# Performance work log

Measured on AMD Instinct MI355X. Metric: run time of the kernel, lower is better.

Reference implementation:

```python
import jax, jax.numpy as jnp
import numpy as np
from jax import lax

N = 100000
IN_C, HID, OUT_C = 512, 256, 128
K_STEPS = 10
ALPHA = 0.1
RES_ALPHA = 1.0
LN_EPS = 1e-5


def layer_norm(h, g, b):
    mu = jnp.mean(h, axis=-1, keepdims=True)
    var = jnp.mean(jnp.square(h - mu), axis=-1, keepdims=True)
    return (h - mu) * lax.rsqrt(var + LN_EPS) * g + b


def appnp(h, src, dst):
    # add self loops
    loop = jnp.arange(N, dtype=src.dtype)
    s = jnp.concatenate([src, loop])
    d = jnp.concatenate([dst, loop])
    ew = jnp.ones(s.shape[0], h.dtype)
    deg = jax.ops.segment_sum(ew, d, num_segments=N)
    dis = jnp.where(deg > 0, lax.rsqrt(jnp.maximum(deg, 1e-12)), 0.0)
    norm = dis[s] * ew * dis[d]  # [E+N]
    h0 = h
    def step(carry, _):
        msg = norm[:, None] * carry[s]                      # gather [E+N, C]
        agg = jax.ops.segment_sum(msg, d, num_segments=N)    # scatter-add
        return (1.0 - ALPHA) * agg + ALPHA * h0, None
    h, _ = lax.scan(step, h, None, length=K_STEPS)
    return h


def setup_inputs() -> dict:
    key = jax.random.key(0)
    ks = jax.random.split(key, 12)
    def lin(k, fan_in, fan_out):
        bound = 1.0 / np.sqrt(fan_in)
        kw, kb = jax.random.split(k)
        W = jax.random.uniform(kw, (fan_in, fan_out), jnp.float32, -bound, bound)
        b = jax.random.uniform(kb, (fan_out,), jnp.float32, -bound, bound)
        return W, b
    x = jax.random.normal(ks[0], (N, IN_C), jnp.float32)
    edge_index = jax.random.randint(ks[1], (2, 1600000), 0, N, jnp.int32)
    W_in, b_in = lin(ks[2], IN_C, HID)
    W1, b1 = lin(ks[3], HID, HID)
    W2, b2 = lin(ks[4], HID, HID)
    W_out, b_out = lin(ks[5], HID, OUT_C)
    g1 = jnp.ones(HID); be1 = jnp.zeros(HID)
    g2 = jnp.ones(HID); be2 = jnp.zeros(HID)
    return {"x": x, "edge_index": edge_index,
            "W_in": W_in, "b_in": b_in,
            "W1": W1, "b1": b1, "g1": g1, "be1": be1,
            "W2": W2, "b2": b2, "g2": g2, "be2": be2,
            "W_out": W_out, "b_out": b_out}


def reference(x, edge_index, W_in, b_in, W1, b1, g1, be1, W2, b2, g2, be2, W_out, b_out):
    # MLP with residual blocks (eval mode: no dropout)
    h = x @ W_in + b_in
    for (W, b, g, be) in ((W1, b1, g1, be1), (W2, b2, g2, be2)):
        identity = h
        h = layer_norm(h @ W + b, g, be)
        h = RES_ALPHA * h + (1.0 - RES_ALPHA) * identity
        h = jax.nn.relu(h)
    h = h @ W_out + b_out
    # APPNP propagation
    return appnp(h, edge_index[0], edge_index[1])
```

## Files before the change

kernel.cpp:

```cpp
#include <hip/hip_runtime.h>

typedef unsigned short u16;
typedef unsigned long long u64;
typedef __attribute__((ext_vector_type(8))) short bfrag;
typedef __attribute__((ext_vector_type(4))) float f32x4;

__device__ inline float b2f(u16 u) {
    union { unsigned int i; float f; } v; v.i = ((unsigned int)u) << 16; return v.f;
}
__device__ inline u16 f2b(float f) {
    union { float f; unsigned int u; } v; v.f = f;
    unsigned int r = v.u + 0x7fffu + ((v.u >> 16) & 1u);
    return (u16)(r >> 16);
}
__device__ inline float ldF(const void* p, size_t i, bool bf) {
    return bf ? b2f(((const u16*)p)[i]) : ((const float*)p)[i];
}
__device__ inline void gload_lds16(const void* g, void* l) {
    __builtin_amdgcn_global_load_lds((const __attribute__((address_space(1))) unsigned int*)g,
                                     (__attribute__((address_space(3))) unsigned int*)l, 16, 0, 0);
}

__global__ void detect_k(const unsigned int* __restrict__ g1w, int* flag) {
    if (blockIdx.x == 0 && threadIdx.x == 0)
        *flag = (g1w[0] == 0x3F803F80u) ? 1 : 0;
}

__global__ void wt_k(const void* __restrict__ W, u16* __restrict__ Wt, int K, int NC,
                     const int* __restrict__ flagp) {
    int i = blockIdx.x * 256 + threadIdx.x;
    if (i >= K * NC) return;
    int k = i / NC, nn = i - k * NC;
    u16 v = (*flagp) ? ((const u16*)W)[i] : f2b(((const float*)W)[i]);
    Wt[(size_t)nn * K + k] = v;
}

template<int K, bool A_DUAL>
__global__ __launch_bounds__(256) void gemm_bt(const void* __restrict__ Ain, const u16* __restrict__ Bt,
                                               const void* __restrict__ bias, u16* __restrict__ C,
                                               int M, int NC, const int* __restrict__ flagp) {
    const int BM = 128, BN = 128, BK = 32;
    const int KI = K / BK;
    __shared__ u16 sh[32768];
    const bool bf = (*flagp != 0);
    int nt = NC / BN;

    int nwg = gridDim.x, bid = blockIdx.x;
    int qc = nwg >> 3, rc = nwg & 7;
    int xcd = bid & 7, off = bid >> 3;
    int swz = (xcd < rc ? xcd * (qc + 1) : rc * (qc + 1) + (xcd - rc) * qc) + off;
    int m0 = (swz / nt) * BM;
    int n0 = (swz % nt) * BN;

    int t = threadIdx.x;
    int lane = t & 63, wave = t >> 6;
    int wm = (wave >> 1) * 64, wn = (wave & 1) * 64;

    f32x4 acc[4][4];
#pragma unroll
    for (int i = 0; i < 4; i++)
#pragma unroll
        for (int j = 0; j < 4; j++) acc[i][j] = (f32x4){0.f, 0.f, 0.f, 0.f};

    char* shb = (char*)sh;
    auto ldsA = [&](int bufi) { return shb + bufi * 8192; };
    auto ldsB = [&](int bufi) { return shb + 32768 + bufi * 8192; };

    auto stageAsync = [&](int bufi, int kk) {
#pragma unroll
        for (int q = 0; q < 2; ++q) {
            int idx = q * 256 + t, row = idx >> 2, cb = (idx & 3) * 16;
            int ra = m0 + row; ra = ra < M ? ra : M - 1;
            gload_lds16((const char*)Bt + ((size_t)(n0 + row) * K + kk) * 2 + cb,
                        ldsB(bufi) + q * 4096 + wave * 1024);
            gload_lds16((const char*)Ain + ((size_t)ra * K + kk) * 2 + cb,
                        ldsA(bufi) + q * 4096 + wave * 1024);
        }
    };
    auto stageB = [&](int bufi, int kk) {
#pragma unroll
        for (int q = 0; q < 2; ++q) {
            int idx = q * 256 + t, row = idx >> 2, cb = (idx & 3) * 16;
            gload_lds16((const char*)Bt + ((size_t)(n0 + row) * K + kk) * 2 + cb,
                        ldsB(bufi) + q * 4096 + wave * 1024);
        }
    };
    float4 fr[2][2];
    auto loadA32 = [&](int kk) {
#pragma unroll
        for (int q = 0; q < 2; ++q) {
            int idx = q * 256 + t, row = idx >> 2, cf = (idx & 3) * 8;
            int ra = m0 + row; ra = ra < M ? ra : M - 1;
            const float* g = (const float*)Ain + (size_t)ra * K + kk + cf;
            fr[q][0] = *(const float4*)g;
            fr[q][1] = *(const float4*)(g + 4);
        }
    };
    auto writeA32 = [&](int bufi) {
#pragma unroll
        for (int q = 0; q < 2; ++q) {
            ushort4 o0, o1;
            o0.x = f2b(fr[q][0].x); o0.y = f2b(fr[q][0].y); o0.z = f2b(fr[q][0].z); o0.w = f2b(fr[q][0].w);
            o1.x = f2b(fr[q][1].x); o1.y = f2b(fr[q][1].y); o1.z = f2b(fr[q][1].z); o1.w = f2b(fr[q][1].w);
            char* la = ldsA(bufi) + q * 4096 + wave * 1024 + lane * 16;
            *(ushort4*)la = o0;
            *(ushort4*)(la + 8) = o1;
        }
    };

    int r16 = lane & 15, q8 = (lane >> 4) * 8;
    const bool a32 = A_DUAL && !bf;

    if (!a32) {
        stageAsync(0, 0);
        stageAsync(1, BK);
#pragma unroll
        for (int ki = 0; ki < KI; ++ki) {
            if (ki + 2 < KI) stageAsync((ki + 2) & 3, (ki + 2) * BK);
            if (ki + 2 < KI)       asm volatile("s_waitcnt vmcnt(8)" ::: "memory");
            else if (ki + 2 == KI) asm volatile("s_waitcnt vmcnt(4)" ::: "memory");
            else                   asm volatile("s_waitcnt vmcnt(0)" ::: "memory");
            asm volatile("s_barrier" ::: "memory");
            const u16* Ac = (const u16*)ldsA(ki & 3);
            const u16* Bc = (const u16*)ldsB(ki & 3);
            bfrag a[4], b[4];
#pragma unroll
            for (int i = 0; i < 4; i++) a[i] = *(const bfrag*)&Ac[(wm + i * 16 + r16) * BK + q8];
#pragma unroll
            for (int j = 0; j < 4; j++) b[j] = *(const bfrag*)&Bc[(wn + j * 16 + r16) * BK + q8];
#pragma unroll
            for (int i = 0; i < 4; i++)
#pragma unroll
                for (int j = 0; j < 4; j++)
                    acc[i][j] = __builtin_amdgcn_mfma_f32_16x16x32_bf16(a[i], b[j], acc[i][j], 0, 0, 0);
        }
    } else {
        loadA32(0);
        stageB(0, 0);
        writeA32(0);
        __syncthreads();
        int cur = 0;
        for (int k0 = 0; k0 < K; k0 += BK) {
            bool next = (k0 + BK < K);
            if (next) { loadA32(k0 + BK); stageB(cur ^ 1, k0 + BK); }
            const u16* Ac = (const u16*)ldsA(cur);
            const u16* Bc = (const u16*)ldsB(cur);
            bfrag a[4], b[4];
#pragma unroll
            for (int i = 0; i < 4; i++) a[i] = *(const bfrag*)&Ac[(wm + i * 16 + r16) * BK + q8];
#pragma unroll
            for (int j = 0; j < 4; j++) b[j] = *(const bfrag*)&Bc[(wn + j * 16 + r16) * BK + q8];
#pragma unroll
            for (int i = 0; i < 4; i++)
#pragma unroll
                for (int j = 0; j < 4; j++)
                    acc[i][j] = __builtin_amdgcn_mfma_f32_16x16x32_bf16(a[i], b[j], acc[i][j], 0, 0, 0);
            if (next) writeA32(cur ^ 1);
            __syncthreads();
            cur ^= 1;
        }
    }
    __syncthreads();

    int q4 = (lane >> 4) * 4;
#pragma unroll
    for (int j = 0; j < 4; j++) {
        int cg = n0 + wn + j * 16 + r16;
        float bvv = ldF(bias, cg, bf);
        int colb = (wn + j * 16 + r16) * 2;
#pragma unroll
        for (int i = 0; i < 4; i++) {
#pragma unroll
            for (int rr = 0; rr < 4; rr++) {
                int row = wm + i * 16 + q4 + rr;
                int sw = colb ^ (((row >> 2) & 3) << 5);
                *(u16*)(shb + row * 256 + sw) = f2b(acc[i][j][rr] + bvv);
            }
        }
    }
    __syncthreads();
#pragma unroll
    for (int pass = 0; pass < 8; ++pass) {
        int u = pass * 256 + t;
        int row = u >> 4;
        int cb = (u & 15) * 16;
        int sw = cb ^ (((row >> 2) & 3) << 5);
        uint4 vv = *(const uint4*)(shb + row * 256 + sw);
        int rg = m0 + row;
        if (rg < M)
            *(uint4*)((char*)C + ((size_t)rg * NC + n0) * 2 + cb) = vv;
    }
}

__global__ __launch_bounds__(256) void ln_relu_k(const u16* __restrict__ T, const void* __restrict__ g,
                                                 const void* __restrict__ be, u16* __restrict__ out,
                                                 int M, const int* __restrict__ flagp) {
    const bool bf = (*flagp != 0);
    int wave = threadIdx.x >> 6, lane = threadIdx.x & 63;
    int row = blockIdx.x * 4 + wave;
    if (row >= M) return;
    const ushort4 xq = *(const ushort4*)(T + (size_t)row * 256 + lane * 4);
    float x0 = b2f(xq.x), x1 = b2f(xq.y), x2 = b2f(xq.z), x3 = b2f(xq.w);
    float s = x0 + x1 + x2 + x3;
    for (int o = 32; o > 0; o >>= 1) s += __shfl_xor(s, o);
    float mu = s * (1.0f / 256.0f);
    float d0 = x0 - mu, d1 = x1 - mu, d2 = x2 - mu, d3 = x3 - mu;
    float q = d0 * d0 + d1 * d1 + d2 * d2 + d3 * d3;
    for (int o = 32; o > 0; o >>= 1) q += __shfl_xor(q, o);
    float rs = rsqrtf(q * (1.0f / 256.0f) + 1e-5f);
    int c0 = lane * 4;
    float y0 = fmaxf(d0 * rs * ldF(g, c0 + 0, bf) + ldF(be, c0 + 0, bf), 0.f);
    float y1 = fmaxf(d1 * rs * ldF(g, c0 + 1, bf) + ldF(be, c0 + 1, bf), 0.f);
    float y2 = fmaxf(d2 * rs * ldF(g, c0 + 2, bf) + ldF(be, c0 + 2, bf), 0.f);
    float y3 = fmaxf(d3 * rs * ldF(g, c0 + 3, bf) + ldF(be, c0 + 3, bf), 0.f);
    ushort4 o4; o4.x = f2b(y0); o4.y = f2b(y1); o4.z = f2b(y2); o4.w = f2b(y3);
    *(ushort4*)(out + (size_t)row * 256 + c0) = o4;
}

__global__ void deg_count(const int* __restrict__ dst, int* deg, int E) {
    int i = blockIdx.x * 256 + threadIdx.x;
    if (i < E) atomicAdd(&deg[dst[i]], 1);
}
__global__ void dis_k(const int* __restrict__ deg, float* dis, int n) {
    int i = blockIdx.x * 256 + threadIdx.x;
    if (i < n) dis[i] = rsqrtf((float)(deg[i] + 1));
}

__global__ void scan_block(const int* __restrict__ deg, int* rowptr, int* bsum, int n) {
    __shared__ int sh[256];
    int t = threadIdx.x, i = blockIdx.x * 256 + t;
    int v = (i < n) ? deg[i] + 1 : 0;
    sh[t] = v; __syncthreads();
    for (int o = 1; o < 256; o <<= 1) {
        int x = (t >= o) ? sh[t - o] : 0;
        __syncthreads();
        sh[t] += x;
        __syncthreads();
    }
    if (i < n) rowptr[i] = sh[t] - v;
    if (t == 255) bsum[blockIdx.x] = sh[t];
}
__global__ void scan_sums(int* bsum, int nb) {
    __shared__ int sh[512];
    int t = threadIdx.x;
    int v = (t < nb) ? bsum[t] : 0;
    sh[t] = v; __syncthreads();
    for (int o = 1; o < 512; o <<= 1) {
        int x = (t >= o) ? sh[t - o] : 0;
        __syncthreads();
        sh[t] += x;
        __syncthreads();
    }
    if (t < nb) bsum[t] = sh[t] - v;
}
__global__ void scan_add(int* rowptr, const int* __restrict__ bsum, int n, int total) {
    int i = blockIdx.x * 256 + threadIdx.x;
    if (i < n) rowptr[i] += bsum[blockIdx.x];
    if (i == 0) rowptr[n] = total;
}
__global__ void fill_k(const int* __restrict__ src, const int* __restrict__ dst,
                       const int* __restrict__ rowptr, int* cursor, const float* __restrict__ dis,
                       int2* __restrict__ epack, int E, int n) {
    int i = blockIdx.x * 256 + threadIdx.x;
    if (i >= E + n) return;
    int s, d;
    if (i < E) { s = src[i]; d = dst[i]; }
    else       { s = d = i - E; }
    int p = rowptr[d] + atomicAdd(&cursor[d], 1);
    float wv = dis[s] * dis[d];
    u64 e = ((u64)__float_as_uint(wv) << 32) | (unsigned int)s;
    __builtin_nontemporal_store(e, (u64*)&epack[p]);
}

__global__ __launch_bounds__(256) void prop_k(const u16* __restrict__ curb, const u16* __restrict__ h0b,
                                              const int* __restrict__ rowptr, const int2* __restrict__ epack,
                                              u16* __restrict__ outB, void* __restrict__ outD,
                                              const int* __restrict__ flagp, int n) {
    int wave = threadIdx.x >> 6, lane = threadIdx.x & 63;
    int node = blockIdx.x * 4 + wave;
    if (node >= n) return;
    int p0 = rowptr[node], p1 = rowptr[node + 1];
    float ax = 0.f, ay = 0.f;
    for (int p = p0; p < p1; p += 64) {
        int cnt = p1 - p; if (cnt > 64) cnt = 64;
        int sj = 0; float wj = 0.f;
        if (lane < cnt) {
            u64 e = __builtin_nontemporal_load((const u64*)(epack + p + lane));
            sj = (int)(unsigned int)e;
            wj = __uint_as_float((unsigned int)(e >> 32));
        }
        int j = 0;
        for (; j + 16 <= cnt; j += 16) {
            float ww[16]; unsigned int v[16];
#pragma unroll
            for (int u = 0; u < 16; ++u) {
                int ss = __shfl(sj, j + u);
                ww[u] = __shfl(wj, j + u);
                v[u] = *(const unsigned int*)(curb + (size_t)ss * 128 + 2 * lane);
            }
#pragma unroll
            for (int u = 0; u < 16; ++u) {
                ax = fmaf(ww[u], b2f((u16)(v[u] & 0xffffu)), ax);
                ay = fmaf(ww[u], b2f((u16)(v[u] >> 16)), ay);
            }
        }
        for (; j < cnt; j += 8) {
            float ww[8]; unsigned int v[8];
#pragma unroll
            for (int u = 0; u < 8; ++u) {
                int jj = j + u;
                bool ok = jj < cnt;
                if (!ok) jj = cnt - 1;
                int ss = __shfl(sj, jj);
                float w2 = __shfl(wj, jj);
                ww[u] = ok ? w2 : 0.f;
                v[u] = *(const unsigned int*)(curb + (size_t)ss * 128 + 2 * lane);
            }
#pragma unroll
            for (int u = 0; u < 8; ++u) {
                ax = fmaf(ww[u], b2f((u16)(v[u] & 0xffffu)), ax);
                ay = fmaf(ww[u], b2f((u16)(v[u] >> 16)), ay);
            }
        }
    }
    unsigned int hp = __builtin_nontemporal_load((const unsigned int*)h0b + (size_t)node * 64 + lane);
    float rx = 0.9f * ax + 0.1f * b2f((u16)(hp & 0xffffu));
    float ry = 0.9f * ay + 0.1f * b2f((u16)(hp >> 16));
    unsigned int pk = ((unsigned int)f2b(ry) << 16) | (unsigned int)f2b(rx);
    if (outB) {
        __builtin_nontemporal_store(pk, (unsigned int*)outB + (size_t)node * 64 + lane);
    } else if (*flagp) {
        __builtin_nontemporal_store(pk, (unsigned int*)outD + (size_t)node * 64 + lane);
    } else {
        u64 o = ((u64)__float_as_uint(ry) << 32) | __float_as_uint(rx);
        __builtin_nontemporal_store(o, (u64*)((float*)outD + (size_t)node * 128 + 2 * lane));
    }
}

extern "C" void kernel_launch(void* const* d_in, const int* in_sizes, int n_in,
                              void* d_out, int out_size, void* d_ws, size_t ws_size,
                              hipStream_t stream) {
    const int N = in_sizes[0] / 512;
    const int E = in_sizes[1] / 2;
    const void* x    = d_in[0];
    const int*  ei   = (const int*)d_in[1];
    const void* Win  = d_in[2];
    const void* bin  = d_in[3];
    const void* W1   = d_in[4];
    const void* b1   = d_in[5];
    const void* g1   = d_in[6];
    const void* be1  = d_in[7];
    const void* W2   = d_in[8];
    const void* b2   = d_in[9];
    const void* g2   = d_in[10];
    const void* be2  = d_in[11];
    const void* Wout = d_in[12];
    const void* bout = d_in[13];
    (void)n_in; (void)out_size; (void)ws_size;

    char* w = (char*)d_ws;
    auto alloc = [&](size_t b) { char* p = w; w += (b + 255) & ~(size_t)255; return p; };
    char*  buf0 = alloc((size_t)N * 512 * 2);
    char*  actAraw = alloc((size_t)N * 256 * 2);
    u16* WtIn  = (u16*)alloc((size_t)512 * 256 * 2);
    u16* Wt1   = (u16*)alloc((size_t)256 * 256 * 2);
    u16* Wt2   = (u16*)alloc((size_t)256 * 256 * 2);
    u16* WtOut = (u16*)alloc((size_t)256 * 128 * 2);
    int*   deg    = (int*)alloc((size_t)N * 4);
    float* dis    = (float*)alloc((size_t)N * 4);
    int*   rowptr = (int*)alloc((size_t)(N + 1) * 4);
    int*   cursor = (int*)alloc((size_t)N * 4);
    int*   bsum   = (int*)alloc(512 * 4);
    int*   flag   = (int*)alloc(256);
    u16*   Tb  = (u16*)buf0;
    u16*   h0b = (u16*)buf0;
    u16*   cA  = (u16*)(buf0 + (size_t)N * 128 * 2);
    u16*   cB  = (u16*)(buf0 + (size_t)N * 128 * 4);
    u16*   actA  = (u16*)actAraw;
    int2*  epack = (int2*)actAraw;

    detect_k<<<1, 64, 0, stream>>>((const unsigned int*)g1, flag);

    wt_k<<<(512 * 256 + 255) / 256, 256, 0, stream>>>(Win,  WtIn,  512, 256, flag);
    wt_k<<<(256 * 256 + 255) / 256, 256, 0, stream>>>(W1,   Wt1,   256, 256, flag);
    wt_k<<<(256 * 256 + 255) / 256, 256, 0, stream>>>(W2,   Wt2,   256, 256, flag);
    wt_k<<<(256 * 128 + 255) / 256, 256, 0, stream>>>(Wout, WtOut, 256, 128, flag);

    int mt = (N + 127) / 128;
    gemm_bt<512, true ><<<mt * 2, 256, 0, stream>>>(x,    WtIn,  bin,  actA, N, 256, flag);
    gemm_bt<256, false><<<mt * 2, 256, 0, stream>>>(actA, Wt1,   b1,   Tb,   N, 256, flag);
    ln_relu_k<<<(N + 3) / 4, 256, 0, stream>>>(Tb, g1, be1, actA, N, flag);
    gemm_bt<256, false><<<mt * 2, 256, 0, stream>>>(actA, Wt2,   b2,   Tb,   N, 256, flag);
    ln_relu_k<<<(N + 3) / 4, 256, 0, stream>>>(Tb, g2, be2, actA, N, flag);
    gemm_bt<256, false><<<mt * 1, 256, 0, stream>>>(actA, WtOut, bout, h0b,  N, 128, flag);

    hipMemsetAsync(deg, 0, (size_t)N * 4, stream);
    deg_count<<<(E + 255) / 256, 256, 0, stream>>>(ei + E, deg, E);
    dis_k    <<<(N + 255) / 256, 256, 0, stream>>>(deg, dis, N);
    int nb = (N + 255) / 256;
    scan_block<<<nb, 256, 0, stream>>>(deg, rowptr, bsum, N);
    scan_sums<<<1, 512, 0, stream>>>(bsum, nb);
    scan_add<<<nb, 256, 0, stream>>>(rowptr, bsum, N, E + N);
    hipMemsetAsync(cursor, 0, (size_t)N * 4, stream);
    fill_k<<<(E + N + 255) / 256, 256, 0, stream>>>(ei, ei + E, rowptr, cursor, dis, epack, E, N);

    const u16* cur = h0b;
    for (int it = 0; it < 10; ++it) {
        bool last = (it == 9);
        u16* o = (it & 1) ? cB : cA;
        prop_k<<<(N + 3) / 4, 256, 0, stream>>>(cur, h0b, rowptr, epack,
                                                last ? nullptr : o,
                                                last ? d_out : nullptr, flag, N);
        cur = o;
    }
}
```

Baseline: 1.366 ms.

## Store GEMM A operands in tile-blocked bf16 layout with a pre-transpose kernel

```diff
diff --git a/kernel.cpp b/kernel.cpp
--- a/kernel.cpp
+++ b/kernel.cpp
@@ -24,6 +24,44 @@
 __global__ void detect_k(const unsigned int* __restrict__ g1w, int* flag) {
     if (blockIdx.x == 0 && threadIdx.x == 0)
         *flag = (g1w[0] == 0x3F803F80u) ? 1 : 0;
+}
+
+__global__ __launch_bounds__(256) void xpose_k(const void* __restrict__ x, u16* __restrict__ xB,
+                                               int N_, const int* __restrict__ flagp) {
+    __shared__ u16 xs[32 * 516];
+    const bool bf = (*flagp != 0);
+    int r0 = blockIdx.x * 32;
+    if (r0 >= N_) return;
+    int t = threadIdx.x;
+    if (bf) {
+#pragma unroll
+        for (int p = 0; p < 8; ++p) {
+            int u = p * 256 + t;
+            int ri = u >> 6, cb = (u & 63) * 16;
+            uint4 v = *(const uint4*)((const char*)x + ((size_t)(r0 + ri)) * 1024 + cb);
+            *(uint4*)((char*)xs + ri * 1032 + cb) = v;
+        }
+    } else {
+#pragma unroll
+        for (int p = 0; p < 16; ++p) {
+            int u = p * 256 + t;
+            int ri = u >> 7, cf = (u & 127) * 4;
+            float4 v = *(const float4*)((const float*)x + ((size_t)(r0 + ri)) * 512 + cf);
+            ushort4 o; o.x = f2b(v.x); o.y = f2b(v.y); o.z = f2b(v.z); o.w = f2b(v.w);
+            *(ushort4*)((char*)xs + ri * 1032 + cf * 2) = o;
+        }
+    }
+    __syncthreads();
+    int tile = r0 >> 7, rbase = r0 & 127;
+    size_t tb = (size_t)tile * (16 * 8192);
+#pragma unroll
+    for (int p = 0; p < 8; ++p) {
+        int u = p * 256 + t;
+        int s = u >> 7, w = u & 127;
+        int ri = w >> 2, c = (w & 3) * 16;
+        uint4 v = *(const uint4*)((char*)xs + ri * 1032 + s * 64 + c);
+        *(uint4*)((char*)xB + tb + (size_t)s * 8192 + (rbase + ri) * 64 + c) = v;
+    }
 }
 
 __global__ void wt_k(const void* __restrict__ W, u16* __restrict__ Wt, int K, int NC,
@@ -35,8 +73,8 @@
     Wt[(size_t)nn * K + k] = v;
 }
 
-template<int K, bool A_DUAL>
-__global__ __launch_bounds__(256) void gemm_bt(const void* __restrict__ Ain, const u16* __restrict__ Bt,
+template<int K, bool OUT_BLK>
+__global__ __launch_bounds__(256) void gemm_bt(const u16* __restrict__ Ablk, const u16* __restrict__ Bt,
                                                const void* __restrict__ bias, u16* __restrict__ C,
                                                int M, int NC, const int* __restrict__ flagp) {
     const int BM = 128, BN = 128, BK = 32;
@@ -66,99 +104,43 @@
     auto ldsA = [&](int bufi) { return shb + bufi * 8192; };
     auto ldsB = [&](int bufi) { return shb + 32768 + bufi * 8192; };
 
-    auto stageAsync = [&](int bufi, int kk) {
+    const size_t tileBase = (size_t)(m0 >> 7) * ((size_t)(K >> 5) * 8192);
+    auto stageAsync = [&](int bufi, int k0) {
+        size_t abase = tileBase + (size_t)(k0 >> 5) * 8192;
 #pragma unroll
         for (int q = 0; q < 2; ++q) {
-            int idx = q * 256 + t, row = idx >> 2, cb = (idx & 3) * 16;
-            int ra = m0 + row; ra = ra < M ? ra : M - 1;
-            gload_lds16((const char*)Bt + ((size_t)(n0 + row) * K + kk) * 2 + cb,
+            int idx = q * 256 + t;
+            gload_lds16((const char*)Ablk + abase + (size_t)idx * 16,
+                        ldsA(bufi) + q * 4096 + wave * 1024);
+            int row = idx >> 2, cb = (idx & 3) * 16;
+            gload_lds16((const char*)Bt + ((size_t)(n0 + row) * K + k0) * 2 + cb,
                         ldsB(bufi) + q * 4096 + wave * 1024);
-            gload_lds16((const char*)Ain + ((size_t)ra * K + kk) * 2 + cb,
-                        ldsA(bufi) + q * 4096 + wave * 1024);
         }
     };
-    auto stageB = [&](int bufi, int kk) {
-#pragma unroll
-        for (int q = 0; q < 2; ++q) {
-            int idx = q * 256 + t, row = idx >> 2, cb = (idx & 3) * 16;
-            gload_lds16((const char*)Bt + ((size_t)(n0 + row) * K + kk) * 2 + cb,
-                        ldsB(bufi) + q * 4096 + wave * 1024);
-        }
-    };
-    float4 fr[2][2];
-    auto loadA32 = [&](int kk) {
-#pragma unroll
-        for (int q = 0; q < 2; ++q) {
-            int idx = q * 256 + t, row = idx >> 2, cf = (idx & 3) * 8;
-            int ra = m0 + row; ra = ra < M ? ra : M - 1;
-            const float* g = (const float*)Ain + (size_t)ra * K + kk + cf;
-            fr[q][0] = *(const float4*)g;
-            fr[q][1] = *(const float4*)(g + 4);
-        }
-    };
-    auto writeA32 = [&](int bufi) {
-#pragma unroll
-        for (int q = 0; q < 2; ++q) {
-            ushort4 o0, o1;
-            o0.x = f2b(fr[q][0].x); o0.y = f2b(fr[q][0].y); o0.z = f2b(fr[q][0].z); o0.w = f2b(fr[q][0].w);
-            o1.x = f2b(fr[q][1].x); o1.y = f2b(fr[q][1].y); o1.z = f2b(fr[q][1].z); o1.w = f2b(fr[q][1].w);
-            char* la = ldsA(bufi) + q * 4096 + wave * 1024 + lane * 16;
-            *(ushort4*)la = o0;
-            *(ushort4*)(la + 8) = o1;
-        }
-    };
 
     int r16 = lane & 15, q8 = (lane >> 4) * 8;
-    const bool a32 = A_DUAL && !bf;
-
-    if (!a32) {
-        stageAsync(0, 0);
-        stageAsync(1, BK);
-#pragma unroll
-        for (int ki = 0; ki < KI; ++ki) {
-            if (ki + 2 < KI) stageAsync((ki + 2) & 3, (ki + 2) * BK);
-            if (ki + 2 < KI)       asm volatile("s_waitcnt vmcnt(8)" ::: "memory");
-            else if (ki + 2 == KI) asm volatile("s_waitcnt vmcnt(4)" ::: "memory");
-            else                   asm volatile("s_waitcnt vmcnt(0)" ::: "memory");
-            asm volatile("s_barrier" ::: "memory");
-            const u16* Ac = (const u16*)ldsA(ki & 3);
-            const u16* Bc = (const u16*)ldsB(ki & 3);
-            bfrag a[4], b[4];
-#pragma unroll
-            for (int i = 0; i < 4; i++) a[i] = *(const bfrag*)&Ac[(wm + i * 16 + r16) * BK + q8];
-#pragma unroll
-            for (int j = 0; j < 4; j++) b[j] = *(const bfrag*)&Bc[(wn + j * 16 + r16) * BK + q8];
-#pragma unroll
-            for (int i = 0; i < 4; i++)
-#pragma unroll
-                for (int j = 0; j < 4; j++)
-                    acc[i][j] = __builtin_amdgcn_mfma_f32_16x16x32_bf16(a[i], b[j], acc[i][j], 0, 0, 0);
-        }
-    } else {
-        loadA32(0);
-        stageB(0, 0);
-        writeA32(0);
-        __syncthreads();
-        int cur = 0;
-        for (int k0 = 0; k0 < K; k0 += BK) {
-            bool next = (k0 + BK < K);
-            if (next) { loadA32(k0 + BK); stageB(cur ^ 1, k0 + BK); }
-            const u16* Ac = (const u16*)ldsA(cur);
-            const u16* Bc = (const u16*)ldsB(cur);
-            bfrag a[4], b[4];
-#pragma unroll
-            for (int i = 0; i < 4; i++) a[i] = *(const bfrag*)&Ac[(wm + i * 16 + r16) * BK + q8];
-#pragma unroll
-            for (int j = 0; j < 4; j++) b[j] = *(const bfrag*)&Bc[(wn + j * 16 + r16) * BK + q8];
-#pragma unroll
-            for (int i = 0; i < 4; i++)
-#pragma unroll
-                for (int j = 0; j < 4; j++)
-                    acc[i][j] = __builtin_amdgcn_mfma_f32_16x16x32_bf16(a[i], b[j], acc[i][j], 0, 0, 0);
-            if (next) writeA32(cur ^ 1);
-            __syncthreads();
-            cur ^= 1;
-        }
+
+    stageAsync(0, 0);
+    stageAsync(1, BK);
+#pragma unroll
+    for (int ki = 0; ki < KI; ++ki) {
+        if (ki + 2 < KI) stageAsync((ki + 2) & 3, (ki + 2) * BK);
+        if (ki + 2 < KI)       asm volatile("s_waitcnt vmcnt(8)" ::: "memory");
+        else if (ki + 2 == KI) asm volatile("s_waitcnt vmcnt(4)" ::: "memory");
+        else                   asm volatile("s_waitcnt vmcnt(0)" ::: "memory");
+        asm volatile("s_barrier" ::: "memory");
+        const u16* Ac = (const u16*)ldsA(ki & 3);
+        const u16* Bc = (const u16*)ldsB(ki & 3);
+        bfrag a[4], b[4];
+#pragma unroll
+        for (int i = 0; i < 4; i++) a[i] = *(const bfrag*)&Ac[(wm + i * 16 + r16) * BK + q8];
+#pragma unroll
+        for (int j = 0; j < 4; j++) b[j] = *(const bfrag*)&Bc[(wn + j * 16 + r16) * BK + q8];
+#pragma unroll
+        for (int i = 0; i < 4; i++)
+#pragma unroll
+            for (int j = 0; j < 4; j++)
+                acc[i][j] = __builtin_amdgcn_mfma_f32_16x16x32_bf16(a[i], b[j], acc[i][j], 0, 0, 0);
     }
     __syncthreads();
 
@@ -179,16 +161,31 @@
         }
     }
     __syncthreads();
-#pragma unroll
-    for (int pass = 0; pass < 8; ++pass) {
-        int u = pass * 256 + t;
-        int row = u >> 4;
-        int cb = (u & 15) * 16;
-        int sw = cb ^ (((row >> 2) & 3) << 5);
-        uint4 vv = *(const uint4*)(shb + row * 256 + sw);
-        int rg = m0 + row;
-        if (rg < M)
-            *(uint4*)((char*)C + ((size_t)rg * NC + n0) * 2 + cb) = vv;
+    if (OUT_BLK) {
+        size_t tb = (size_t)(m0 >> 7) * 65536 + (size_t)(n0 >> 5) * 8192;
+#pragma unroll
+        for (int pass = 0; pass < 8; ++pass) {
+            int u = pass * 256 + t;
+            int s = u >> 9;
+            int ri = (u >> 2) & 127;
+            int cb = (u & 3) * 16;
+            int sw = (s * 64 + cb) ^ (((ri >> 2) & 3) << 5);
+            uint4 vv = *(const uint4*)(shb + ri * 256 + sw);
+            if (m0 + ri < M)
+                *(uint4*)((char*)C + tb + (size_t)s * 8192 + ri * 64 + cb) = vv;
+        }
+    } else {
+#pragma unroll
+        for (int pass = 0; pass < 8; ++pass) {
+            int u = pass * 256 + t;
+            int row = u >> 4;
+            int cb = (u & 15) * 16;
+            int sw = cb ^ (((row >> 2) & 3) << 5);
+            uint4 vv = *(const uint4*)(shb + row * 256 + sw);
+            int rg = m0 + row;
+            if (rg < M)
+                *(uint4*)((char*)C + ((size_t)rg * NC + n0) * 2 + cb) = vv;
+        }
     }
 }
 
@@ -214,7 +211,9 @@
     float y2 = fmaxf(d2 * rs * ldF(g, c0 + 2, bf) + ldF(be, c0 + 2, bf), 0.f);
     float y3 = fmaxf(d3 * rs * ldF(g, c0 + 3, bf) + ldF(be, c0 + 3, bf), 0.f);
     ushort4 o4; o4.x = f2b(y0); o4.y = f2b(y1); o4.z = f2b(y2); o4.w = f2b(y3);
-    *(ushort4*)(out + (size_t)row * 256 + c0) = o4;
+    size_t tb = (size_t)(row >> 7) * 65536;
+    int ri = row & 127;
+    *(ushort4*)((char*)out + tb + (size_t)(lane >> 3) * 8192 + ri * 64 + (lane & 7) * 8) = o4;
 }
 
 __global__ void deg_count(const int* __restrict__ dst, int* deg, int E) {
@@ -358,10 +357,11 @@
     const void* bout = d_in[13];
     (void)n_in; (void)out_size; (void)ws_size;
 
+    const int NT = (N + 127) / 128;
     char* w = (char*)d_ws;
     auto alloc = [&](size_t b) { char* p = w; w += (b + 255) & ~(size_t)255; return p; };
-    char*  buf0 = alloc((size_t)N * 512 * 2);
-    char*  actAraw = alloc((size_t)N * 256 * 2);
+    char*  reg0 = alloc((size_t)NT * 16 * 8192);
+    char*  reg1 = alloc((size_t)NT * 8 * 8192);
     u16* WtIn  = (u16*)alloc((size_t)512 * 256 * 2);
     u16* Wt1   = (u16*)alloc((size_t)256 * 256 * 2);
     u16* Wt2   = (u16*)alloc((size_t)256 * 256 * 2);
@@ -372,27 +372,28 @@
     int*   cursor = (int*)alloc((size_t)N * 4);
     int*   bsum   = (int*)alloc(512 * 4);
     int*   flag   = (int*)alloc(256);
-    u16*   Tb  = (u16*)buf0;
-    u16*   h0b = (u16*)buf0;
-    u16*   cA  = (u16*)(buf0 + (size_t)N * 128 * 2);
-    u16*   cB  = (u16*)(buf0 + (size_t)N * 128 * 4);
-    u16*   actA  = (u16*)actAraw;
-    int2*  epack = (int2*)actAraw;
+    u16*   xB    = (u16*)reg0;
+    u16*   Tb    = (u16*)reg0;
+    u16*   h0b   = (u16*)(reg0 + (size_t)N * 256 * 2);
+    u16*   cA    = (u16*)(reg0 + (size_t)N * 384 * 2);
+    u16*   actAB = (u16*)reg1;
+    int2*  epack = (int2*)reg1;
+    u16*   cB    = (u16*)(reg1 + 16 * 1024 * 1024);
 
     detect_k<<<1, 64, 0, stream>>>((const unsigned int*)g1, flag);
 
+    xpose_k<<<(N + 31) / 32, 256, 0, stream>>>(x, xB, N, flag);
     wt_k<<<(512 * 256 + 255) / 256, 256, 0, stream>>>(Win,  WtIn,  512, 256, flag);
     wt_k<<<(256 * 256 + 255) / 256, 256, 0, stream>>>(W1,   Wt1,   256, 256, flag);
     wt_k<<<(256 * 256 + 255) / 256, 256, 0, stream>>>(W2,   Wt2,   256, 256, flag);
     wt_k<<<(256 * 128 + 255) / 256, 256, 0, stream>>>(Wout, WtOut, 256, 128, flag);
 
-    int mt = (N + 127) / 128;
-    gemm_bt<512, true ><<<mt * 2, 256, 0, stream>>>(x,    WtIn,  bin,  actA, N, 256, flag);
-    gemm_bt<256, false><<<mt * 2, 256, 0, stream>>>(actA, Wt1,   b1,   Tb,   N, 256, flag);
-    ln_relu_k<<<(N + 3) / 4, 256, 0, stream>>>(Tb, g1, be1, actA, N, flag);
-    gemm_bt<256, false><<<mt * 2, 256, 0, stream>>>(actA, Wt2,   b2,   Tb,   N, 256, flag);
-    ln_relu_k<<<(N + 3) / 4, 256, 0, stream>>>(Tb, g2, be2, actA, N, flag);
-    gemm_bt<256, false><<<mt * 1, 256, 0, stream>>>(actA, WtOut, bout, h0b,  N, 128, flag);
+    gemm_bt<512, true ><<<NT * 2, 256, 0, stream>>>(xB,    WtIn,  bin,  actAB, N, 256, flag);
+    gemm_bt<256, false><<<NT * 2, 256, 0, stream>>>(actAB, Wt1,   b1,   Tb,    N, 256, flag);
+    ln_relu_k<<<(N + 3) / 4, 256, 0, stream>>>(Tb, g1, be1, actAB, N, flag);
+    gemm_bt<256, false><<<NT * 2, 256, 0, stream>>>(actAB, Wt2,   b2,   Tb,    N, 256, flag);
+    ln_relu_k<<<(N + 3) / 4, 256, 0, stream>>>(Tb, g2, be2, actAB, N, flag);
+    gemm_bt<256, false><<<NT * 1, 256, 0, stream>>>(actAB, WtOut, bout, h0b,   N, 128, flag);
 
     hipMemsetAsync(deg, 0, (size_t)N * 4, stream);
     deg_count<<<(E + 255) / 256, 256, 0, stream>>>(ei + E, deg, E);
```

Result: slower. 1.418 ms (+3.8%).
